# Kernel tuning notes

Hardware: AMD Instinct MI355X
Metric: run time of the kernel (lower is better)

The kernel has to match this reference:

```python
import jax, jax.numpy as jnp
import numpy as np

B, T, N, FIN, D, LAG = 8, 64, 128, 64, 64, 8


def setup_inputs() -> dict:
    key = jax.random.key(0)
    ks = jax.random.split(key, 9)
    s_in = 0.05
    X = jax.random.normal(ks[0], (B, T, N, FIN), jnp.float32)
    Wq = jax.random.normal(ks[1], (FIN, D), jnp.float32) * s_in
    bq = jnp.zeros((D,), jnp.float32)
    Wk = jax.random.normal(ks[2], (FIN, D), jnp.float32) * s_in
    bk = jnp.zeros((D,), jnp.float32)
    Wv = jax.random.normal(ks[3], (FIN, D), jnp.float32) * s_in
    bv = jnp.zeros((D,), jnp.float32)
    Wo = jax.random.normal(ks[4], (2 * D, D), jnp.float32) * s_in
    bo = jnp.zeros((D,), jnp.float32)
    return {"X": X, "Wq": Wq, "bq": bq, "Wk": Wk, "bk": bk,
            "Wv": Wv, "bv": bv, "Wo": Wo, "bo": bo}


def reference(X, Wq, bq, Wk, bk, Wv, bv, Wo, bo):
    relu = jax.nn.relu
    Q = relu(jnp.einsum('btnf,fd->btnd', X, Wq) + bq)  # [B,T,N,D]
    K = relu(jnp.einsum('btnf,fd->btnd', X, Wk) + bk)
    V = relu(jnp.einsum('btnf,fd->btnd', X, Wv) + bv)

    pad = LAG - 1
    # Zero-pad time axis at the front so negative lags gather zeros
    # (faithful to the torch code: padded slots score 0 and still get
    #  softmax mass exp(0), they are NOT masked with -inf).
    Kp = jnp.pad(K, ((0, 0), (pad, 0), (0, 0), (0, 0)))
    Vp = jnp.pad(V, ((0, 0), (pad, 0), (0, 0), (0, 0)))
    # t_idx[t, l] = (t - l) + pad  -> index into padded time axis
    t_idx = jnp.arange(T)[:, None] - jnp.arange(LAG)[None, :] + pad  # [T,LAG]
    Kl = Kp[:, t_idx]  # [B,T,LAG,N,D]
    Vl = Vp[:, t_idx]  # [B,T,LAG,N,D]

    scale = 1.0 / jnp.sqrt(jnp.float32(D))
    scores = jnp.einsum('btnd,btlmd->btnlm', Q, Kl) * scale  # [B,T,N,LAG,N]
    scores = scores.reshape(B, T, N, LAG * N)
    w = jax.nn.softmax(scores, axis=-1)  # softmax over full lag-window KV
    agg = jnp.einsum('btnk,btkd->btnd', w, Vl.reshape(B, T, LAG * N, D))

    h = jnp.concatenate([Q, agg], axis=-1)  # [B,T,N,2D]
    out = relu(jnp.einsum('btnc,cd->btnd', h, Wo) + bo)
    # dropout is identity in eval mode
    return out
```

## Files before the change

kernel.cpp:

```cpp
#include <hip/hip_runtime.h>
#include <stdint.h>


typedef __bf16 bf16x8 __attribute__((ext_vector_type(8)));
typedef float f32x4 __attribute__((ext_vector_type(4)));

#define MFMA16(a, b, c) __builtin_amdgcn_mfma_f32_16x16x32_bf16((a), (b), (c), 0, 0, 0)

__device__ __forceinline__ unsigned short f2bf(float f) {
    union { float f; unsigned u; } v; v.f = f;
    unsigned r = v.u + 0x7FFFu + ((v.u >> 16) & 1u);
    return (unsigned short)(r >> 16);
}
__device__ __forceinline__ unsigned cvtpk(float lo, float hi) {
    unsigned r;
    asm("v_cvt_pk_bf16_f32 %0, %1, %2" : "=v"(r) : "v"(lo), "v"(hi));
    return r;
}
__device__ __forceinline__ f32x4 fzero4() {
    f32x4 z; z[0] = 0.f; z[1] = 0.f; z[2] = 0.f; z[3] = 0.f; return z;
}

__global__ __launch_bounds__(256) void qkv_kernel(
    const float* __restrict__ X,
    const float* __restrict__ Wq, const float* __restrict__ bq,
    const float* __restrict__ Wk, const float* __restrict__ bk,
    const float* __restrict__ Wv, const float* __restrict__ bv,
    unsigned short* __restrict__ Qo, unsigned short* __restrict__ Ko,
    unsigned short* __restrict__ Vt)
{
    __shared__ __align__(16) unsigned short WTl[192 * 64];
    unsigned char* wtb = (unsigned char*)WTl;

    const int tid = threadIdx.x;
    for (int i = tid; i < 4096; i += 256) {
        int f = i >> 6, c = i & 63;
        float wq_ = Wq[f * 64 + c], wk_ = Wk[f * 64 + c], wv_ = Wv[f * 64 + c];
        int c0 = c,        b0 = (c0 * 128 + f * 2) ^ ((c0 & 7) << 4);
        int c1 = c + 64,   b1 = (c1 * 128 + f * 2) ^ ((c1 & 7) << 4);
        int c2 = c + 128,  b2 = (c2 * 128 + f * 2) ^ ((c2 & 7) << 4);
        *(unsigned short*)(wtb + b0) = f2bf(wq_);
        *(unsigned short*)(wtb + b1) = f2bf(wk_);
        *(unsigned short*)(wtb + b2) = f2bf(wv_);
    }
    __syncthreads();

    const int lane = tid & 63, wv_id = tid >> 6;
    const int cl = lane & 15, g = lane >> 4;
    const size_t row0 = (size_t)blockIdx.x * 64 + wv_id * 16;
    const int bt = (int)(row0 >> 7);
    const int nb = (int)(row0 & 127);

    bf16x8 xf[2];
    {
        const float* xp = X + (row0 + cl) * 64;
#pragma unroll
        for (int kk = 0; kk < 2; ++kk) {
            float4 a = *(const float4*)(xp + kk * 32 + g * 8);
            float4 b = *(const float4*)(xp + kk * 32 + g * 8 + 4);
            unsigned u[4];
            u[0] = cvtpk(a.x, a.y); u[1] = cvtpk(a.z, a.w);
            u[2] = cvtpk(b.x, b.y); u[3] = cvtpk(b.z, b.w);
            xf[kk] = *(bf16x8*)u;
        }
    }

    f32x4 accq[4], acck[4], accv[4];
#pragma unroll
    for (int i = 0; i < 4; ++i) { accq[i] = fzero4(); acck[i] = fzero4(); accv[i] = fzero4(); }

#pragma unroll
    for (int kk = 0; kk < 2; ++kk) {
#pragma unroll
        for (int dt = 0; dt < 4; ++dt) {
            int cq = dt * 16 + cl;
            bf16x8 wqf = *(const bf16x8*)(wtb + ((cq * 128 + (kk * 32 + g * 8) * 2) ^ ((cq & 7) << 4)));
            accq[dt] = MFMA16(wqf, xf[kk], accq[dt]);
            int ck = 64 + dt * 16 + cl;
            bf16x8 wkf = *(const bf16x8*)(wtb + ((ck * 128 + (kk * 32 + g * 8) * 2) ^ ((ck & 7) << 4)));
            acck[dt] = MFMA16(wkf, xf[kk], acck[dt]);
            int cv = 128 + dt * 16 + cl;
            bf16x8 wvf = *(const bf16x8*)(wtb + ((cv * 128 + (kk * 32 + g * 8) * 2) ^ ((cv & 7) << 4)));
            accv[dt] = MFMA16(xf[kk], wvf, accv[dt]);
        }
    }

#pragma unroll
    for (int dt = 0; dt < 4; ++dt) {
        float q0 = fmaxf(accq[dt][0] + bq[dt * 16 + g * 4 + 0], 0.f);
        float q1 = fmaxf(accq[dt][1] + bq[dt * 16 + g * 4 + 1], 0.f);
        float q2 = fmaxf(accq[dt][2] + bq[dt * 16 + g * 4 + 2], 0.f);
        float q3 = fmaxf(accq[dt][3] + bq[dt * 16 + g * 4 + 3], 0.f);
        uint2 qp; qp.x = cvtpk(q0, q1); qp.y = cvtpk(q2, q3);
        *(uint2*)(Qo + (row0 + cl) * 64 + dt * 16 + g * 4) = qp;

        float k0 = fmaxf(acck[dt][0] + bk[dt * 16 + g * 4 + 0], 0.f);
        float k1 = fmaxf(acck[dt][1] + bk[dt * 16 + g * 4 + 1], 0.f);
        float k2 = fmaxf(acck[dt][2] + bk[dt * 16 + g * 4 + 2], 0.f);
        float k3 = fmaxf(acck[dt][3] + bk[dt * 16 + g * 4 + 3], 0.f);
        uint2 kp; kp.x = cvtpk(k0, k1); kp.y = cvtpk(k2, k3);
        *(uint2*)(Ko + (row0 + cl) * 64 + dt * 16 + g * 4) = kp;

        int d = dt * 16 + cl;
        float bvv = bv[d];
        float v0 = fmaxf(accv[dt][0] + bvv, 0.f);
        float v1 = fmaxf(accv[dt][1] + bvv, 0.f);
        float v2 = fmaxf(accv[dt][2] + bvv, 0.f);
        float v3 = fmaxf(accv[dt][3] + bvv, 0.f);
        uint2 vp; vp.x = cvtpk(v0, v1); vp.y = cvtpk(v2, v3);
        *(uint2*)(Vt + (size_t)bt * 8192 + d * 128 + nb + g * 4) = vp;
    }
}

__global__ __launch_bounds__(512, 4) void attn_kernel(
    const unsigned short* __restrict__ Qg,
    const unsigned short* __restrict__ Kg,
    const unsigned short* __restrict__ Vt,
    const float* __restrict__ Wo,
    const float* __restrict__ bo,
    float* __restrict__ Out)
{
    __shared__ __align__(16) unsigned char ldsK[16384];
    __shared__ __align__(16) unsigned char ldsV[16384];
    __shared__ __align__(16) unsigned char ldsP[32768];
    __shared__ float lsumBuf[128];

    const int tid = threadIdx.x;
    const int lane = tid & 63, wv = tid >> 6;
    const int cl = lane & 15, g = lane >> 4;
    const int bid = blockIdx.x;
    const int bt = (bid & 7) * 64 + (bid >> 3);
    const int t = bt & 63;
    const int wq0 = wv * 16;

    bf16x8 qf[2];
    {
        const unsigned short* qp = Qg + ((size_t)bt * 128 + wq0 + cl) * 64;
        qf[0] = *(const bf16x8*)(qp + g * 8);
        qf[1] = *(const bf16x8*)(qp + 32 + g * 8);
    }

    f32x4 o[4];
#pragma unroll
    for (int ni = 0; ni < 4; ++ni) o[ni] = fzero4();
    float lsum = 0.f;

    const int lg0 = (t < 7) ? (7 - t) : 0;

    uint4 kreg[2], vreg[2];
    {
        const uint4* kp = (const uint4*)(Kg + (size_t)(bt - 7 + lg0) * 8192);
        const uint4* vp = (const uint4*)(Vt + (size_t)(bt - 7 + lg0) * 8192);
        kreg[0] = kp[tid]; kreg[1] = kp[tid + 512];
        vreg[0] = vp[tid]; vreg[1] = vp[tid + 512];
    }

    for (int lg = lg0; lg < 8; ++lg) {
        __syncthreads();
        {
#pragma unroll
            for (int j = 0; j < 2; ++j) {
                int i = tid + j * 512;
                int key = i >> 3, d0 = (i & 7) * 8;
                *(uint4*)(ldsK + ((key * 128 + d0 * 2) ^ ((key & 7) << 4))) = kreg[j];
                int d = i >> 4, n0 = (i & 15) * 8;
                *(uint4*)(ldsV + ((d * 256 + n0 * 2) ^ ((d & 7) << 4))) = vreg[j];
            }
        }
        if (lg < 7) {
            const uint4* kp = (const uint4*)(Kg + (size_t)(bt - 6 + lg) * 8192);
            const uint4* vp = (const uint4*)(Vt + (size_t)(bt - 6 + lg) * 8192);
            kreg[0] = kp[tid]; kreg[1] = kp[tid + 512];
            vreg[0] = vp[tid]; vreg[1] = vp[tid + 512];
        }
        __syncthreads();

        f32x4 s[8];
#pragma unroll
        for (int ki = 0; ki < 8; ++ki) s[ki] = fzero4();
#pragma unroll
        for (int ki = 0; ki < 8; ++ki) {
            int key = ki * 16 + cl;
#pragma unroll
            for (int kk = 0; kk < 2; ++kk) {
                bf16x8 kf = *(const bf16x8*)(ldsK + ((key * 128 + (kk * 32 + g * 8) * 2) ^ ((key & 7) << 4)));
                s[ki] = MFMA16(kf, qf[kk], s[ki]);
            }
        }

        const int q = wq0 + cl;
#pragma unroll
        for (int ki = 0; ki < 8; ++ki) {
            float p0 = __expf(s[ki][0] * 0.125f);
            float p1 = __expf(s[ki][1] * 0.125f);
            float p2 = __expf(s[ki][2] * 0.125f);
            float p3 = __expf(s[ki][3] * 0.125f);
            lsum += (p0 + p1) + (p2 + p3);
            uint2 pk; pk.x = cvtpk(p0, p1); pk.y = cvtpk(p2, p3);
            *(uint2*)(ldsP + ((q * 256 + (ki * 16 + g * 4) * 2) ^ ((q & 7) << 4))) = pk;
        }

#pragma unroll
        for (int kk2 = 0; kk2 < 4; ++kk2) {
            bf16x8 pf = *(const bf16x8*)(ldsP + ((q * 256 + (kk2 * 32 + g * 8) * 2) ^ ((q & 7) << 4)));
#pragma unroll
            for (int ni = 0; ni < 4; ++ni) {
                int d = ni * 16 + cl;
                bf16x8 vf = *(const bf16x8*)(ldsV + ((d * 256 + (kk2 * 32 + g * 8) * 2) ^ ((d & 7) << 4)));
                o[ni] = MFMA16(pf, vf, o[ni]);
            }
        }
    }

    float ls = lsum;
    ls += __shfl_xor(ls, 16, 64);
    ls += __shfl_xor(ls, 32, 64);
    if (t < 7) ls += 128.0f * (float)(7 - t);
    if (g == 0) lsumBuf[wq0 + cl] = ls;
    __syncthreads();

    float inv[4];
#pragma unroll
    for (int r = 0; r < 4; ++r) inv[r] = 1.0f / lsumBuf[wq0 + g * 4 + r];
#pragma unroll
    for (int ni = 0; ni < 4; ++ni)
#pragma unroll
        for (int r = 0; r < 4; ++r) {
            int qq = wq0 + g * 4 + r;
            int d = ni * 16 + cl;
            *(unsigned short*)(ldsK + ((qq * 128 + d * 2) ^ ((qq & 7) << 4))) =
                f2bf(o[ni][r] * inv[r]);
        }

    for (int i = tid; i < 8192; i += 512) {
        int c = i >> 6, d = i & 63;
        *(unsigned short*)(ldsV + ((d * 256 + c * 2) ^ ((d & 7) << 4))) = f2bf(Wo[c * 64 + d]);
    }
    __syncthreads();

    f32x4 h2[4];
#pragma unroll
    for (int ni = 0; ni < 4; ++ni) h2[ni] = fzero4();
#pragma unroll
    for (int kk = 0; kk < 4; ++kk) {
        bf16x8 ha;
        if (kk < 2) {
            ha = qf[kk];
        } else {
            int qq = wq0 + cl;
            ha = *(const bf16x8*)(ldsK + ((qq * 128 + ((kk - 2) * 32 + g * 8) * 2) ^ ((qq & 7) << 4)));
        }
#pragma unroll
        for (int ni = 0; ni < 4; ++ni) {
            int dd = ni * 16 + cl;
            bf16x8 wb = *(const bf16x8*)(ldsV + ((dd * 256 + (kk * 32 + g * 8) * 2) ^ ((dd & 7) << 4)));
            h2[ni] = MFMA16(ha, wb, h2[ni]);
        }
    }
#pragma unroll
    for (int ni = 0; ni < 4; ++ni) {
        float b = bo[ni * 16 + cl];
#pragma unroll
        for (int r = 0; r < 4; ++r) {
            float v = h2[ni][r] + b;
            v = v > 0.f ? v : 0.f;
            Out[((size_t)bt * 128 + wq0 + g * 4 + r) * 64 + ni * 16 + cl] = v;
        }
    }
}

extern "C" void kernel_launch(void* const* d_in, const int* in_sizes, int n_in,
                              void* d_out, int out_size, void* d_ws, size_t ws_size,
                              hipStream_t stream) {
    const float* X  = (const float*)d_in[0];
    const float* Wq = (const float*)d_in[1];
    const float* bq = (const float*)d_in[2];
    const float* Wk = (const float*)d_in[3];
    const float* bk = (const float*)d_in[4];
    const float* Wv = (const float*)d_in[5];
    const float* bv = (const float*)d_in[6];
    const float* Wo = (const float*)d_in[7];
    const float* bo = (const float*)d_in[8];
    float* Out = (float*)d_out;

    unsigned short* Qw = (unsigned short*)d_ws;
    unsigned short* Kw = Qw + (size_t)65536 * 64;
    unsigned short* Vw = Kw + (size_t)65536 * 64;

    hipLaunchKernelGGL(qkv_kernel, dim3(1024), dim3(256), 0, stream,
                       X, Wq, bq, Wk, bk, Wv, bv, Qw, Kw, Vw);
    hipLaunchKernelGGL(attn_kernel, dim3(512), dim3(512), 0, stream,
                       Qw, Kw, Vw, Wo, bo, Out);
}
```

Baseline: 153.4 us.

## Pre-transpose weights to bf16 in a prep kernel; read directly in qkv/attn

```diff
diff --git a/kernel.cpp b/kernel.cpp
--- a/kernel.cpp
+++ b/kernel.cpp
@@ -21,33 +21,37 @@
     f32x4 z; z[0] = 0.f; z[1] = 0.f; z[2] = 0.f; z[3] = 0.f; return z;
 }
 
+__global__ __launch_bounds__(256) void prep_kernel(
+    const float* __restrict__ Wq, const float* __restrict__ Wk,
+    const float* __restrict__ Wv, const float* __restrict__ Wo,
+    unsigned short* __restrict__ WqT, unsigned short* __restrict__ WkT,
+    unsigned short* __restrict__ WvT, unsigned short* __restrict__ WoT)
+{
+    __shared__ float lds[128][65];
+    const int b = blockIdx.x, tid = threadIdx.x;
+    const float* src = (b == 0) ? Wq : (b == 1) ? Wk : (b == 2) ? Wv : Wo;
+    unsigned short* dst = (b == 0) ? WqT : (b == 1) ? WkT : (b == 2) ? WvT : WoT;
+    const int n = (b == 3) ? 8192 : 4096;
+    for (int i = tid; i < n; i += 256) lds[i >> 6][i & 63] = src[i];
+    __syncthreads();
+    if (b == 3) {
+        for (int i = tid; i < 8192; i += 256) { int d = i >> 7, r = i & 127; dst[i] = f2bf(lds[r][d]); }
+    } else {
+        for (int i = tid; i < 4096; i += 256) { int d = i >> 6, r = i & 63;  dst[i] = f2bf(lds[r][d]); }
+    }
+}
+
 __global__ __launch_bounds__(256) void qkv_kernel(
     const float* __restrict__ X,
-    const float* __restrict__ Wq, const float* __restrict__ bq,
-    const float* __restrict__ Wk, const float* __restrict__ bk,
-    const float* __restrict__ Wv, const float* __restrict__ bv,
+    const unsigned short* __restrict__ WqT, const unsigned short* __restrict__ WkT,
+    const unsigned short* __restrict__ WvT,
+    const float* __restrict__ bq, const float* __restrict__ bk, const float* __restrict__ bv,
     unsigned short* __restrict__ Qo, unsigned short* __restrict__ Ko,
     unsigned short* __restrict__ Vt)
 {
-    __shared__ __align__(16) unsigned short WTl[192 * 64];
-    unsigned char* wtb = (unsigned char*)WTl;
-
-    const int tid = threadIdx.x;
-    for (int i = tid; i < 4096; i += 256) {
-        int f = i >> 6, c = i & 63;
-        float wq_ = Wq[f * 64 + c], wk_ = Wk[f * 64 + c], wv_ = Wv[f * 64 + c];
-        int c0 = c,        b0 = (c0 * 128 + f * 2) ^ ((c0 & 7) << 4);
-        int c1 = c + 64,   b1 = (c1 * 128 + f * 2) ^ ((c1 & 7) << 4);
-        int c2 = c + 128,  b2 = (c2 * 128 + f * 2) ^ ((c2 & 7) << 4);
-        *(unsigned short*)(wtb + b0) = f2bf(wq_);
-        *(unsigned short*)(wtb + b1) = f2bf(wk_);
-        *(unsigned short*)(wtb + b2) = f2bf(wv_);
-    }
-    __syncthreads();
-
-    const int lane = tid & 63, wv_id = tid >> 6;
+    const int tid = threadIdx.x, lane = tid & 63, w = tid >> 6;
     const int cl = lane & 15, g = lane >> 4;
-    const size_t row0 = (size_t)blockIdx.x * 64 + wv_id * 16;
+    const size_t row0 = (size_t)blockIdx.x * 64 + w * 16;
     const int bt = (int)(row0 >> 7);
     const int nb = (int)(row0 & 127);
 
@@ -71,52 +75,52 @@
 
 #pragma unroll
     for (int kk = 0; kk < 2; ++kk) {
+        const int wo = kk * 32 + g * 8;
 #pragma unroll
         for (int dt = 0; dt < 4; ++dt) {
-            int cq = dt * 16 + cl;
-            bf16x8 wqf = *(const bf16x8*)(wtb + ((cq * 128 + (kk * 32 + g * 8) * 2) ^ ((cq & 7) << 4)));
+            const int rw = (dt * 16 + cl) * 64 + wo;
+            bf16x8 wqf = *(const bf16x8*)(WqT + rw);
+            bf16x8 wkf = *(const bf16x8*)(WkT + rw);
+            bf16x8 wvf = *(const bf16x8*)(WvT + rw);
             accq[dt] = MFMA16(wqf, xf[kk], accq[dt]);
-            int ck = 64 + dt * 16 + cl;
-            bf16x8 wkf = *(const bf16x8*)(wtb + ((ck * 128 + (kk * 32 + g * 8) * 2) ^ ((ck & 7) << 4)));
             acck[dt] = MFMA16(wkf, xf[kk], acck[dt]);
-            int cv = 128 + dt * 16 + cl;
-            bf16x8 wvf = *(const bf16x8*)(wtb + ((cv * 128 + (kk * 32 + g * 8) * 2) ^ ((cv & 7) << 4)));
             accv[dt] = MFMA16(xf[kk], wvf, accv[dt]);
         }
     }
 
 #pragma unroll
     for (int dt = 0; dt < 4; ++dt) {
-        float q0 = fmaxf(accq[dt][0] + bq[dt * 16 + g * 4 + 0], 0.f);
-        float q1 = fmaxf(accq[dt][1] + bq[dt * 16 + g * 4 + 1], 0.f);
-        float q2 = fmaxf(accq[dt][2] + bq[dt * 16 + g * 4 + 2], 0.f);
-        float q3 = fmaxf(accq[dt][3] + bq[dt * 16 + g * 4 + 3], 0.f);
+        float4 bq4 = *(const float4*)(bq + dt * 16 + g * 4);
+        float q0 = fmaxf(accq[dt][0] + bq4.x, 0.f);
+        float q1 = fmaxf(accq[dt][1] + bq4.y, 0.f);
+        float q2 = fmaxf(accq[dt][2] + bq4.z, 0.f);
+        float q3 = fmaxf(accq[dt][3] + bq4.w, 0.f);
         uint2 qp; qp.x = cvtpk(q0, q1); qp.y = cvtpk(q2, q3);
         *(uint2*)(Qo + (row0 + cl) * 64 + dt * 16 + g * 4) = qp;
 
-        float k0 = fmaxf(acck[dt][0] + bk[dt * 16 + g * 4 + 0], 0.f);
-        float k1 = fmaxf(acck[dt][1] + bk[dt * 16 + g * 4 + 1], 0.f);
-        float k2 = fmaxf(acck[dt][2] + bk[dt * 16 + g * 4 + 2], 0.f);
-        float k3 = fmaxf(acck[dt][3] + bk[dt * 16 + g * 4 + 3], 0.f);
+        float4 bk4 = *(const float4*)(bk + dt * 16 + g * 4);
+        float k0 = fmaxf(acck[dt][0] + bk4.x, 0.f);
+        float k1 = fmaxf(acck[dt][1] + bk4.y, 0.f);
+        float k2 = fmaxf(acck[dt][2] + bk4.z, 0.f);
+        float k3 = fmaxf(acck[dt][3] + bk4.w, 0.f);
         uint2 kp; kp.x = cvtpk(k0, k1); kp.y = cvtpk(k2, k3);
         *(uint2*)(Ko + (row0 + cl) * 64 + dt * 16 + g * 4) = kp;
 
-        int d = dt * 16 + cl;
-        float bvv = bv[d];
+        float bvv = bv[dt * 16 + cl];
         float v0 = fmaxf(accv[dt][0] + bvv, 0.f);
         float v1 = fmaxf(accv[dt][1] + bvv, 0.f);
         float v2 = fmaxf(accv[dt][2] + bvv, 0.f);
         float v3 = fmaxf(accv[dt][3] + bvv, 0.f);
         uint2 vp; vp.x = cvtpk(v0, v1); vp.y = cvtpk(v2, v3);
-        *(uint2*)(Vt + (size_t)bt * 8192 + d * 128 + nb + g * 4) = vp;
-    }
-}
-
-__global__ __launch_bounds__(512, 4) void attn_kernel(
+        *(uint2*)(Vt + (size_t)bt * 8192 + (dt * 16 + cl) * 128 + nb + g * 4) = vp;
+    }
+}
+
+__global__ __launch_bounds__(512, 2) void attn_kernel(
     const unsigned short* __restrict__ Qg,
     const unsigned short* __restrict__ Kg,
     const unsigned short* __restrict__ Vt,
-    const float* __restrict__ Wo,
+    const unsigned short* __restrict__ WoT,
     const float* __restrict__ bo,
     float* __restrict__ Out)
 {
@@ -232,9 +236,14 @@
                 f2bf(o[ni][r] * inv[r]);
         }
 
-    for (int i = tid; i < 8192; i += 512) {
-        int c = i >> 6, d = i & 63;
-        *(unsigned short*)(ldsV + ((d * 256 + c * 2) ^ ((d & 7) << 4))) = f2bf(Wo[c * 64 + d]);
+    {
+        const uint4* wo4 = (const uint4*)WoT;
+#pragma unroll
+        for (int j = 0; j < 2; ++j) {
+            int i = tid + j * 512;
+            int d = i >> 4, c0 = (i & 15) * 8;
+            *(uint4*)(ldsV + ((d * 256 + c0 * 2) ^ ((d & 7) << 4))) = wo4[i];
+        }
     }
     __syncthreads();
 
@@ -286,9 +295,16 @@
     unsigned short* Qw = (unsigned short*)d_ws;
     unsigned short* Kw = Qw + (size_t)65536 * 64;
     unsigned short* Vw = Kw + (size_t)65536 * 64;
-
+    unsigned short* Wt  = Vw + (size_t)65536 * 64;
+    unsigned short* WqT = Wt;
+    unsigned short* WkT = Wt + 4096;
+    unsigned short* WvT = Wt + 8192;
+    unsigned short* WoT = Wt + 12288;
+
+    hipLaunchKernelGGL(prep_kernel, dim3(4), dim3(256), 0, stream,
+                       Wq, Wk, Wv, Wo, WqT, WkT, WvT, WoT);
     hipLaunchKernelGGL(qkv_kernel, dim3(1024), dim3(256), 0, stream,
-                       X, Wq, bq, Wk, bk, Wv, bv, Qw, Kw, Vw);
+                       X, WqT, WkT, WvT, bq, bk, bv, Qw, Kw, Vw);
     hipLaunchKernelGGL(attn_kernel, dim3(512), dim3(512), 0, stream,
-                       Qw, Kw, Vw, Wo, bo, Out);
-}
+                       Qw, Kw, Vw, WoT, bo, Out);
+}
```

New measurement: 164.8 us. 7.5% more time.
